# Kernel optimization log

Measured on AMD Instinct MI355X. Metric: run time of the kernel, lower is better.

## Reference

```python
import jax, jax.numpy as jnp
import numpy as np

B, D, NB, BS = 32, 2048, 16, 512  # batch, dim_input=dim_output, n_blocks, block_size; NB*BS*BS == D*D


def setup_inputs() -> dict:
    key = jax.random.key(0)
    k1, k2, k3, k4, k5 = jax.random.split(key, 5)
    x = jax.random.normal(k1, (B, D), dtype=jnp.float32)
    gate_w = jax.random.normal(k2, (D, NB), dtype=jnp.float32) / np.sqrt(D)
    gate_b = jax.random.normal(k3, (NB,), dtype=jnp.float32) * 0.02
    weight = jax.random.normal(k4, (D, D), dtype=jnp.float32) / np.sqrt(D)  # kaiming-uniform-like scale
    bias = jax.random.normal(k5, (D,), dtype=jnp.float32) * (1.0 / np.sqrt(D))
    return {"x": x, "gate_w": gate_w, "gate_b": gate_b, "weight": weight, "bias": bias}


def reference(x, gate_w, gate_b, weight, bias):
    b = x.shape[0]
    k_drop = NB // 2
    # gate network: Linear -> Sigmoid
    g = jax.nn.sigmoid(x @ gate_w + gate_b)  # (b, NB)
    # zero out the k smallest gates per sample (topk largest=False, scatter 0)
    _, drop_idx = jax.lax.top_k(-g, k_drop)  # indices of smallest gates
    rows = jnp.arange(b)[:, None]
    g = g.at[rows, drop_idx].set(0.0)
    # broadcast gates over block-diagonal chunks of weight
    w0 = weight.reshape(NB, BS, BS)
    gw = (g[:, :, None, None] * w0).reshape(b, D, D)  # (b, dim_output, dim_input)
    # batched matvec + bias
    return jnp.einsum('bij,bj->bi', gw, x) + bias
```

## Files before the change

kernel.cpp:

```cpp
#include <hip/hip_runtime.h>
#include <hip/hip_bf16.h>


#define D_DIM 2048
#define B_DIM 32
#define NB_DIM 16
#define KSPLIT 16
#define KCHUNK (D_DIM / KSPLIT)

typedef __attribute__((ext_vector_type(4))) float f32x4;
typedef __attribute__((ext_vector_type(8))) float f32x8;
typedef __attribute__((ext_vector_type(8))) __bf16 bf16x8;

static __device__ __forceinline__ __bf16 f2bf(float f) {
    unsigned u = __builtin_bit_cast(unsigned, f);
    u += 0x7fffu + ((u >> 16) & 1u);
    unsigned short h = (unsigned short)(u >> 16);
    return __builtin_bit_cast(__bf16, h);
}

static __device__ __forceinline__ bf16x8 load_cvt8(const float* p) {
    const f32x8 v = *(const f32x8*)p;
    bf16x8 r;
#pragma unroll
    for (int i = 0; i < 8; ++i) r[i] = f2bf(v[i]);
    return r;
}

__global__ __launch_bounds__(256) void prep_kernel(
    const float* __restrict__ X,
    const float* __restrict__ GW,
    const float* __restrict__ GB,
    const float* __restrict__ bias,
    float* __restrict__ gates,
    float* __restrict__ out)
{
    const int t = threadIdx.x;

    if (blockIdx.x >= B_DIM) {
        const int idx4 = ((blockIdx.x - B_DIM) * 256 + t) * 4;
        const int r = idx4 & (D_DIM - 1);
        *(f32x4*)(out + idx4) = *(const f32x4*)(bias + r);
        return;
    }

    __shared__ float red[NB_DIM][256];
    __shared__ float sg[NB_DIM];
    const int b = blockIdx.x;

    float acc[NB_DIM];
#pragma unroll
    for (int n = 0; n < NB_DIM; ++n) acc[n] = 0.f;

#pragma unroll
    for (int i = 0; i < D_DIM / 256; ++i) {
        const int c = t + i * 256;
        const float xv = X[b * D_DIM + c];
        const float* gw = GW + c * NB_DIM;
#pragma unroll
        for (int n = 0; n < NB_DIM; ++n) acc[n] += xv * gw[n];
    }
#pragma unroll
    for (int n = 0; n < NB_DIM; ++n) red[n][t] = acc[n];
    __syncthreads();
    for (int s = 128; s > 0; s >>= 1) {
        if (t < s) {
#pragma unroll
            for (int n = 0; n < NB_DIM; ++n) red[n][t] += red[n][t + s];
        }
        __syncthreads();
    }
    if (t < NB_DIM) {
        const float v = red[t][0] + GB[t];
        sg[t] = 1.f / (1.f + __expf(-v));
    }
    __syncthreads();
    if (t < NB_DIM) {
        const float g = sg[t];
        int rank = 0;
#pragma unroll
        for (int m = 0; m < NB_DIM; ++m) {
            const float gm = sg[m];
            if (gm < g || (gm == g && m < t)) rank++;
        }
        gates[b * NB_DIM + t] = (rank >= NB_DIM / 2) ? g : 0.f;
    }
}

__global__ __launch_bounds__(256) void gemm_atomic(
    const float* __restrict__ W,
    const float* __restrict__ X,
    const float* __restrict__ gates,
    float* __restrict__ out)
{
    const int bid  = blockIdx.x;
    const int ks   = bid & (KSPLIT - 1);
    const int rg   = bid >> 4;
    const int wave = threadIdx.x >> 6;
    const int lane = threadIdx.x & 63;
    const int l15  = lane & 15;
    const int q    = lane >> 4;

    const int r0 = rg * 64 + wave * 16;
    const int k0 = ks * KCHUNK;

    const float* arow = W + (size_t)(r0 + l15) * D_DIM + k0 + q * 8;
    const float* b0p  = X + (size_t)(l15)      * D_DIM + k0 + q * 8;
    const float* b1p  = X + (size_t)(l15 + 16) * D_DIM + k0 + q * 8;

    f32x4 acc0 = {0.f, 0.f, 0.f, 0.f};
    f32x4 acc1 = {0.f, 0.f, 0.f, 0.f};

#pragma unroll
    for (int kk = 0; kk < KCHUNK / 32; ++kk) {
        const bf16x8 av  = load_cvt8(arow + kk * 32);
        const bf16x8 bv0 = load_cvt8(b0p  + kk * 32);
        const bf16x8 bv1 = load_cvt8(b1p  + kk * 32);
        acc0 = __builtin_amdgcn_mfma_f32_16x16x32_bf16(av, bv0, acc0, 0, 0, 0);
        acc1 = __builtin_amdgcn_mfma_f32_16x16x32_bf16(av, bv1, acc1, 0, 0, 0);
    }

    const int rbase = r0 + q * 4;
    const int nblk  = rbase >> 7;

    const float g0 = gates[l15 * NB_DIM + nblk];
    if (g0 != 0.f) {
        float* o = out + (size_t)l15 * D_DIM + rbase;
#pragma unroll
        for (int i = 0; i < 4; ++i) atomicAdd(o + i, g0 * acc0[i]);
    }
    const float g1 = gates[(l15 + 16) * NB_DIM + nblk];
    if (g1 != 0.f) {
        float* o = out + (size_t)(l15 + 16) * D_DIM + rbase;
#pragma unroll
        for (int i = 0; i < 4; ++i) atomicAdd(o + i, g1 * acc1[i]);
    }
}

extern "C" void kernel_launch(void* const* d_in, const int* in_sizes, int n_in,
                              void* d_out, int out_size, void* d_ws, size_t ws_size,
                              hipStream_t stream) {
    const float* x    = (const float*)d_in[0];
    const float* gw   = (const float*)d_in[1];
    const float* gb   = (const float*)d_in[2];
    const float* w    = (const float*)d_in[3];
    const float* bias = (const float*)d_in[4];
    float* out = (float*)d_out;

    float* gates = (float*)d_ws;

    prep_kernel<<<B_DIM + 64, 256, 0, stream>>>(x, gw, gb, bias, gates, out);
    gemm_atomic<<<32 * KSPLIT, 256, 0, stream>>>(w, x, gates, out);
}
```

Baseline: 97.06 us.

## Fuse gate and GEMM into cooperative kernel with grid sync and in-block reduction

Replaces the two-kernel prep + split-K atomic GEMM with one cooperative kernel of 256 blocks. The first 32 blocks compute the gates, then a grid-wide sync lets every block compute 8 output rows. The K dimension is split across the four waves of a block and reduced in shared memory instead of with global atomics, and bias is added directly, so the separate bias initialisation goes away. This removes a launch, the atomics and the bias prefill. In exchange it adds a grid barrier, uses only half of each MFMA tile (8 useful rows out of 16), and runs far fewer blocks, so the W stream may get less memory-level parallelism.

```diff
diff --git a/kernel.cpp b/kernel.cpp
--- a/kernel.cpp
+++ b/kernel.cpp
@@ -1,12 +1,13 @@
 #include <hip/hip_runtime.h>
 #include <hip/hip_bf16.h>
+#include <hip/hip_cooperative_groups.h>
+
+namespace cg = cooperative_groups;
 
 
 #define D_DIM 2048
 #define B_DIM 32
 #define NB_DIM 16
-#define KSPLIT 16
-#define KCHUNK (D_DIM / KSPLIT)
 
 typedef __attribute__((ext_vector_type(4))) float f32x4;
 typedef __attribute__((ext_vector_type(8))) float f32x8;
@@ -27,114 +28,109 @@
     return r;
 }
 
-__global__ __launch_bounds__(256) void prep_kernel(
+__global__ __launch_bounds__(256) void fused_kernel(
     const float* __restrict__ X,
     const float* __restrict__ GW,
     const float* __restrict__ GB,
+    const float* __restrict__ W,
     const float* __restrict__ bias,
     float* __restrict__ gates,
     float* __restrict__ out)
 {
+    __shared__ float smem[NB_DIM * 256 + NB_DIM];
     const int t = threadIdx.x;
 
-    if (blockIdx.x >= B_DIM) {
-        const int idx4 = ((blockIdx.x - B_DIM) * 256 + t) * 4;
-        const int r = idx4 & (D_DIM - 1);
-        *(f32x4*)(out + idx4) = *(const f32x4*)(bias + r);
-        return;
+    if (blockIdx.x < B_DIM) {
+        float* red = smem;
+        float* sg  = smem + NB_DIM * 256;
+        const int b = blockIdx.x;
+
+        float acc[NB_DIM];
+#pragma unroll
+        for (int n = 0; n < NB_DIM; ++n) acc[n] = 0.f;
+
+#pragma unroll
+        for (int i = 0; i < D_DIM / 256; ++i) {
+            const int c = t + i * 256;
+            const float xv = X[b * D_DIM + c];
+            const float* gw = GW + c * NB_DIM;
+#pragma unroll
+            for (int n = 0; n < NB_DIM; ++n) acc[n] += xv * gw[n];
+        }
+#pragma unroll
+        for (int n = 0; n < NB_DIM; ++n) red[n * 256 + t] = acc[n];
+        __syncthreads();
+        for (int s = 128; s > 0; s >>= 1) {
+            if (t < s) {
+#pragma unroll
+                for (int n = 0; n < NB_DIM; ++n) red[n * 256 + t] += red[n * 256 + t + s];
+            }
+            __syncthreads();
+        }
+        if (t < NB_DIM) {
+            const float v = red[t * 256] + GB[t];
+            sg[t] = 1.f / (1.f + __expf(-v));
+        }
+        __syncthreads();
+        if (t < NB_DIM) {
+            const float g = sg[t];
+            int rank = 0;
+#pragma unroll
+            for (int m = 0; m < NB_DIM; ++m) {
+                const float gm = sg[m];
+                if (gm < g || (gm == g && m < t)) rank++;
+            }
+            gates[b * NB_DIM + t] = (rank >= NB_DIM / 2) ? g : 0.f;
+        }
+        __threadfence();
     }
 
-    __shared__ float red[NB_DIM][256];
-    __shared__ float sg[NB_DIM];
-    const int b = blockIdx.x;
+    cg::this_grid().sync();
 
-    float acc[NB_DIM];
-#pragma unroll
-    for (int n = 0; n < NB_DIM; ++n) acc[n] = 0.f;
-
-#pragma unroll
-    for (int i = 0; i < D_DIM / 256; ++i) {
-        const int c = t + i * 256;
-        const float xv = X[b * D_DIM + c];
-        const float* gw = GW + c * NB_DIM;
-#pragma unroll
-        for (int n = 0; n < NB_DIM; ++n) acc[n] += xv * gw[n];
-    }
-#pragma unroll
-    for (int n = 0; n < NB_DIM; ++n) red[n][t] = acc[n];
-    __syncthreads();
-    for (int s = 128; s > 0; s >>= 1) {
-        if (t < s) {
-#pragma unroll
-            for (int n = 0; n < NB_DIM; ++n) red[n][t] += red[n][t + s];
-        }
-        __syncthreads();
-    }
-    if (t < NB_DIM) {
-        const float v = red[t][0] + GB[t];
-        sg[t] = 1.f / (1.f + __expf(-v));
-    }
-    __syncthreads();
-    if (t < NB_DIM) {
-        const float g = sg[t];
-        int rank = 0;
-#pragma unroll
-        for (int m = 0; m < NB_DIM; ++m) {
-            const float gm = sg[m];
-            if (gm < g || (gm == g && m < t)) rank++;
-        }
-        gates[b * NB_DIM + t] = (rank >= NB_DIM / 2) ? g : 0.f;
-    }
-}
-
-__global__ __launch_bounds__(256) void gemm_atomic(
-    const float* __restrict__ W,
-    const float* __restrict__ X,
-    const float* __restrict__ gates,
-    float* __restrict__ out)
-{
-    const int bid  = blockIdx.x;
-    const int ks   = bid & (KSPLIT - 1);
-    const int rg   = bid >> 4;
-    const int wave = threadIdx.x >> 6;
-    const int lane = threadIdx.x & 63;
+    const int bi   = blockIdx.x;
+    const int r0   = bi * 8;
+    const int nblk = r0 >> 7;
+    const int wave = t >> 6;
+    const int lane = t & 63;
     const int l15  = lane & 15;
     const int q    = lane >> 4;
+    const int row8 = l15 & 7;
 
-    const int r0 = rg * 64 + wave * 16;
-    const int k0 = ks * KCHUNK;
+    const int kb = wave * (D_DIM / 4);
 
-    const float* arow = W + (size_t)(r0 + l15) * D_DIM + k0 + q * 8;
-    const float* b0p  = X + (size_t)(l15)      * D_DIM + k0 + q * 8;
-    const float* b1p  = X + (size_t)(l15 + 16) * D_DIM + k0 + q * 8;
+    const float* arow = W + (size_t)(r0 + row8) * D_DIM + kb + q * 8;
+    const float* b0p  = X + (size_t)(l15)       * D_DIM + kb + q * 8;
+    const float* b1p  = X + (size_t)(l15 + 16)  * D_DIM + kb + q * 8;
 
     f32x4 acc0 = {0.f, 0.f, 0.f, 0.f};
     f32x4 acc1 = {0.f, 0.f, 0.f, 0.f};
 
 #pragma unroll
-    for (int kk = 0; kk < KCHUNK / 32; ++kk) {
-        const bf16x8 av  = load_cvt8(arow + kk * 32);
-        const bf16x8 bv0 = load_cvt8(b0p  + kk * 32);
-        const bf16x8 bv1 = load_cvt8(b1p  + kk * 32);
+    for (int s = 0; s < 16; ++s) {
+        const bf16x8 av  = load_cvt8(arow + s * 32);
+        const bf16x8 bv0 = load_cvt8(b0p  + s * 32);
+        const bf16x8 bv1 = load_cvt8(b1p  + s * 32);
         acc0 = __builtin_amdgcn_mfma_f32_16x16x32_bf16(av, bv0, acc0, 0, 0, 0);
         acc1 = __builtin_amdgcn_mfma_f32_16x16x32_bf16(av, bv1, acc1, 0, 0, 0);
     }
 
-    const int rbase = r0 + q * 4;
-    const int nblk  = rbase >> 7;
+    __syncthreads();
+    float* red = smem;
+    if (q < 2) {
+#pragma unroll
+        for (int i = 0; i < 4; ++i) {
+            red[wave * 256 + (q * 4 + i) * 32 + l15]      = acc0[i];
+            red[wave * 256 + (q * 4 + i) * 32 + 16 + l15] = acc1[i];
+        }
+    }
+    __syncthreads();
 
-    const float g0 = gates[l15 * NB_DIM + nblk];
-    if (g0 != 0.f) {
-        float* o = out + (size_t)l15 * D_DIM + rbase;
-#pragma unroll
-        for (int i = 0; i < 4; ++i) atomicAdd(o + i, g0 * acc0[i]);
-    }
-    const float g1 = gates[(l15 + 16) * NB_DIM + nblk];
-    if (g1 != 0.f) {
-        float* o = out + (size_t)(l15 + 16) * D_DIM + rbase;
-#pragma unroll
-        for (int i = 0; i < 4; ++i) atomicAdd(o + i, g1 * acc1[i]);
-    }
+    const int row = t >> 5;
+    const int b   = t & 31;
+    const float s = red[row * 32 + b] + red[256 + row * 32 + b] +
+                    red[512 + row * 32 + b] + red[768 + row * 32 + b];
+    const float g = gates[b * NB_DIM + nblk];
+    out[(size_t)b * D_DIM + r0 + row] = g * s + bias[r0 + row];
 }
 
 extern "C" void kernel_launch(void* const* d_in, const int* in_sizes, int n_in,
@@ -145,10 +141,11 @@
     const float* gb   = (const float*)d_in[2];
     const float* w    = (const float*)d_in[3];
     const float* bias = (const float*)d_in[4];
-    float* out = (float*)d_out;
-
+    float* out   = (float*)d_out;
     float* gates = (float*)d_ws;
 
-    prep_kernel<<<B_DIM + 64, 256, 0, stream>>>(x, gw, gb, bias, gates, out);
-    gemm_atomic<<<32 * KSPLIT, 256, 0, stream>>>(w, x, gates, out);
+    void* args[] = {(void*)&x, (void*)&gw, (void*)&gb, (void*)&w, (void*)&bias,
+                    (void*)&gates, (void*)&out};
+    hipLaunchCooperativeKernel((const void*)fused_kernel, dim3(256), dim3(256),
+                               args, 0, stream);
 }
```

Result: slower. 125.7 us (+29.5%).

## Replace split-K atomics with in-block K reduction and fused bias epilogue

Applied to the files above, without the earlier changes.

The GEMM is restructured so each block owns four output rows and splits K across its four waves, reducing partial sums in shared memory instead of issuing global atomic adds. Bias is added in the epilogue, which removes the separate bias-initialization blocks, and X is converted to bf16 once in the prep kernel. This removes global atomic contention. In exchange, most of the MFMA lanes compute duplicate rows, which wastes matrix throughput.

```diff
diff --git a/kernel.cpp b/kernel.cpp
--- a/kernel.cpp
+++ b/kernel.cpp
@@ -5,8 +5,6 @@
 #define D_DIM 2048
 #define B_DIM 32
 #define NB_DIM 16
-#define KSPLIT 16
-#define KCHUNK (D_DIM / KSPLIT)
 
 typedef __attribute__((ext_vector_type(4))) float f32x4;
 typedef __attribute__((ext_vector_type(8))) float f32x8;
@@ -31,22 +29,18 @@
     const float* __restrict__ X,
     const float* __restrict__ GW,
     const float* __restrict__ GB,
-    const float* __restrict__ bias,
     float* __restrict__ gates,
-    float* __restrict__ out)
+    __bf16* __restrict__ Xbf)
 {
-    const int t = threadIdx.x;
-
-    if (blockIdx.x >= B_DIM) {
-        const int idx4 = ((blockIdx.x - B_DIM) * 256 + t) * 4;
-        const int r = idx4 & (D_DIM - 1);
-        *(f32x4*)(out + idx4) = *(const f32x4*)(bias + r);
-        return;
-    }
-
     __shared__ float red[NB_DIM][256];
     __shared__ float sg[NB_DIM];
     const int b = blockIdx.x;
+    const int t = threadIdx.x;
+
+    {
+        const int idx = b * D_DIM + t * 8;
+        *(bf16x8*)(Xbf + idx) = load_cvt8(X + idx);
+    }
 
     float acc[NB_DIM];
 #pragma unroll
@@ -87,53 +81,63 @@
     }
 }
 
-__global__ __launch_bounds__(256) void gemm_atomic(
+__global__ __launch_bounds__(256) void gemm_kernel(
     const float* __restrict__ W,
-    const float* __restrict__ X,
+    const __bf16* __restrict__ Xbf,
     const float* __restrict__ gates,
+    const float* __restrict__ bias,
     float* __restrict__ out)
 {
-    const int bid  = blockIdx.x;
-    const int ks   = bid & (KSPLIT - 1);
-    const int rg   = bid >> 4;
-    const int wave = threadIdx.x >> 6;
-    const int lane = threadIdx.x & 63;
+    __shared__ float red[4 * 4 * 32];
+    const int t    = threadIdx.x;
+    const int r0   = blockIdx.x * 4;
+    const int nblk = r0 >> 7;
+    const int wave = t >> 6;
+    const int lane = t & 63;
     const int l15  = lane & 15;
     const int q    = lane >> 4;
 
-    const int r0 = rg * 64 + wave * 16;
-    const int k0 = ks * KCHUNK;
+    const int kb = wave * (D_DIM / 4);
 
-    const float* arow = W + (size_t)(r0 + l15) * D_DIM + k0 + q * 8;
-    const float* b0p  = X + (size_t)(l15)      * D_DIM + k0 + q * 8;
-    const float* b1p  = X + (size_t)(l15 + 16) * D_DIM + k0 + q * 8;
+    const float*  arow = W   + (size_t)(r0 + (l15 & 3)) * D_DIM + kb + q * 8;
+    const __bf16* b0p  = Xbf + (size_t)(l15)            * D_DIM + kb + q * 8;
+    const __bf16* b1p  = Xbf + (size_t)(l15 + 16)       * D_DIM + kb + q * 8;
 
     f32x4 acc0 = {0.f, 0.f, 0.f, 0.f};
     f32x4 acc1 = {0.f, 0.f, 0.f, 0.f};
 
 #pragma unroll
-    for (int kk = 0; kk < KCHUNK / 32; ++kk) {
-        const bf16x8 av  = load_cvt8(arow + kk * 32);
-        const bf16x8 bv0 = load_cvt8(b0p  + kk * 32);
-        const bf16x8 bv1 = load_cvt8(b1p  + kk * 32);
+    for (int s = 0; s < 16; ++s) {
+        const bf16x8 av  = load_cvt8(arow + s * 32);
+        const bf16x8 bv0 = *(const bf16x8*)(b0p + s * 32);
+        const bf16x8 bv1 = *(const bf16x8*)(b1p + s * 32);
         acc0 = __builtin_amdgcn_mfma_f32_16x16x32_bf16(av, bv0, acc0, 0, 0, 0);
         acc1 = __builtin_amdgcn_mfma_f32_16x16x32_bf16(av, bv1, acc1, 0, 0, 0);
     }
 
-    const int rbase = r0 + q * 4;
-    const int nblk  = rbase >> 7;
+    if (q == 0) {
+#pragma unroll
+        for (int i = 0; i < 4; ++i) {
+            red[wave * 128 + i * 32 + l15]      = acc0[i];
+            red[wave * 128 + i * 32 + 16 + l15] = acc1[i];
+        }
+    }
+    __syncthreads();
 
-    const float g0 = gates[l15 * NB_DIM + nblk];
-    if (g0 != 0.f) {
-        float* o = out + (size_t)l15 * D_DIM + rbase;
+    if (t < B_DIM) {
+        const int b = t;
+        f32x4 s;
 #pragma unroll
-        for (int i = 0; i < 4; ++i) atomicAdd(o + i, g0 * acc0[i]);
-    }
-    const float g1 = gates[(l15 + 16) * NB_DIM + nblk];
-    if (g1 != 0.f) {
-        float* o = out + (size_t)(l15 + 16) * D_DIM + rbase;
+        for (int i = 0; i < 4; ++i) {
+            s[i] = red[0 * 128 + i * 32 + b] + red[1 * 128 + i * 32 + b] +
+                   red[2 * 128 + i * 32 + b] + red[3 * 128 + i * 32 + b];
+        }
+        const float g = gates[b * NB_DIM + nblk];
+        const f32x4 bi = *(const f32x4*)(bias + r0);
+        f32x4 y;
 #pragma unroll
-        for (int i = 0; i < 4; ++i) atomicAdd(o + i, g1 * acc1[i]);
+        for (int i = 0; i < 4; ++i) y[i] = g * s[i] + bi[i];
+        *(f32x4*)(out + (size_t)b * D_DIM + r0) = y;
     }
 }
 
@@ -147,8 +151,9 @@
     const float* bias = (const float*)d_in[4];
     float* out = (float*)d_out;
 
-    float* gates = (float*)d_ws;
+    __bf16* Xbf  = (__bf16*)d_ws;
+    float* gates = (float*)((char*)d_ws + (size_t)B_DIM * D_DIM * sizeof(__bf16));
 
-    prep_kernel<<<B_DIM + 64, 256, 0, stream>>>(x, gw, gb, bias, gates, out);
-    gemm_atomic<<<32 * KSPLIT, 256, 0, stream>>>(w, x, gates, out);
+    prep_kernel<<<B_DIM, 256, 0, stream>>>(x, gw, gb, gates, Xbf);
+    gemm_kernel<<<D_DIM / 4, 256, 0, stream>>>(w, Xbf, gates, bias, out);
 }
```

Measured after the change: 91.29 us. 1.06x faster.
